# Kernel optimization log

Measured on AMD Instinct MI355X. Metric: run time of the kernel, lower is better.

## Reference

```python
import jax, jax.numpy as jnp
import numpy as np

N_NODES = 50000
N_EDGES = 800000
F_IN = 64
HIDDEN = 128
HEADS = 4
C = HIDDEN // HEADS  # 32 per-head channels
OUT = 256
N_GRAPHS = 1024
BN_EPS = 1e-5
SLOPE = 0.2  # PyG GATConv leaky_relu negative_slope default


def setup_inputs() -> dict:
    key = jax.random.key(0)
    ks = jax.random.split(key, 16)
    x = jax.random.normal(ks[0], (N_NODES, F_IN), dtype=jnp.float32)
    edge_index = jax.random.randint(ks[1], (2, N_EDGES), 0, N_NODES, dtype=jnp.int64)
    batch = jnp.sort(jax.random.randint(ks[2], (N_NODES,), 0, N_GRAPHS, dtype=jnp.int64))
    s = lambda *d: 1.0 / np.sqrt(d[0])
    W1 = jax.random.normal(ks[3], (F_IN, HIDDEN), dtype=jnp.float32) * s(F_IN)
    att_src1 = jax.random.normal(ks[4], (HEADS, C), dtype=jnp.float32) * s(C)
    att_dst1 = jax.random.normal(ks[5], (HEADS, C), dtype=jnp.float32) * s(C)
    b1 = jnp.zeros((HIDDEN,), jnp.float32)
    W2 = jax.random.normal(ks[6], (HIDDEN, HIDDEN), dtype=jnp.float32) * s(HIDDEN)
    att_src2 = jax.random.normal(ks[7], (HEADS, C), dtype=jnp.float32) * s(C)
    att_dst2 = jax.random.normal(ks[8], (HEADS, C), dtype=jnp.float32) * s(C)
    b2 = jnp.zeros((HIDDEN,), jnp.float32)
    bn1_g = jnp.ones((HIDDEN,), jnp.float32); bn1_b = jnp.zeros((HIDDEN,), jnp.float32)
    bn2_g = jnp.ones((HIDDEN,), jnp.float32); bn2_b = jnp.zeros((HIDDEN,), jnp.float32)
    Wlin = jax.random.normal(ks[9], (HIDDEN, OUT), dtype=jnp.float32) * s(HIDDEN)
    blin = jnp.zeros((OUT,), jnp.float32)
    return {"x": x, "edge_index": edge_index, "batch": batch,
            "W1": W1, "att_src1": att_src1, "att_dst1": att_dst1, "b1": b1,
            "W2": W2, "att_src2": att_src2, "att_dst2": att_dst2, "b2": b2,
            "bn1_g": bn1_g, "bn1_b": bn1_b, "bn2_g": bn2_g, "bn2_b": bn2_b,
            "Wlin": Wlin, "blin": blin}


def _gat_conv(x, W, a_src, a_dst, bias, src, dst):
    # x: [N, Fin] -> h: [N, H, C]
    h = (x @ W).reshape(-1, HEADS, C)
    e_src = jnp.sum(h * a_src, axis=-1)  # [N, H]
    e_dst = jnp.sum(h * a_dst, axis=-1)  # [N, H]
    e = jax.nn.leaky_relu(e_src[src] + e_dst[dst], SLOPE)  # [E, H]
    # scatter-softmax over edges grouped by destination node
    m = jax.ops.segment_max(e, dst, num_segments=N_NODES)
    ex = jnp.exp(e - m[dst])
    denom = jax.ops.segment_sum(ex, dst, num_segments=N_NODES)
    alpha = ex / (denom[dst] + 1e-16)  # [E, H]
    out = jax.ops.segment_sum(alpha[:, :, None] * h[src], dst, num_segments=N_NODES)
    return out.reshape(-1, HEADS * C) + bias


def _batchnorm(x, g, b):
    mu = jnp.mean(x, axis=0)
    var = jnp.var(x, axis=0)
    return (x - mu) * jax.lax.rsqrt(var + BN_EPS) * g + b


def reference(x, edge_index, batch, W1, att_src1, att_dst1, b1, W2, att_src2, att_dst2, b2,
              bn1_g, bn1_b, bn2_g, bn2_b, Wlin, blin):
    # PyG GATConv adds self-loops by default
    ar = jnp.arange(N_NODES, dtype=edge_index.dtype)
    src = jnp.concatenate([edge_index[0], ar])
    dst = jnp.concatenate([edge_index[1], ar])
    h = _gat_conv(x, W1, att_src1, att_dst1, b1, src, dst)
    h = jax.nn.elu(_batchnorm(h, bn1_g, bn1_b))
    h = _gat_conv(h, W2, att_src2, att_dst2, b2, src, dst)
    h = jax.nn.elu(_batchnorm(h, bn2_g, bn2_b))
    # global mean pool per graph
    sums = jax.ops.segment_sum(h, batch, num_segments=N_GRAPHS)
    cnts = jax.ops.segment_sum(jnp.ones((N_NODES,), h.dtype), batch, num_segments=N_GRAPHS)
    pooled = sums / jnp.maximum(cnts, 1.0)[:, None]  # [G, HIDDEN]
    return pooled @ Wlin + blin
```

## Files before the change

### kernel.cpp

```cpp
#include <hip/hip_runtime.h>
#include <hip/hip_bf16.h>
#include <hip/hip_fp16.h>
#include <math.h>

#define N_NODES 50000
#define N_EDGES 800000
#define E_TOT   (N_EDGES + N_NODES)
#define F_IN    64
#define HIDDEN  128
#define HEADS   4
#define OUT_DIM 256
#define N_GRAPHS 1024
#define BN_EPS  1e-5f
#define SLOPE   0.2f

#define SCAN_TILE 2048
#define N_TILES   ((N_NODES + SCAN_TILE - 1) / SCAN_TILE)
#define POOL_NODES 128
#define SCATTER_BLOCKS ((E_TOT + 1023) / 1024)
#define GEMM_BLOCKS    ((N_NODES + 63) / 64)


__global__ void hist_kernel(const int* __restrict__ ei, int* __restrict__ deg) {
    int base = blockIdx.x * blockDim.x * 4 + threadIdx.x;
    #pragma unroll
    for (int u = 0; u < 4; ++u) {
        int i = base + u * 256;
        if (i < E_TOT) {
            int d = (i < N_EDGES) ? ei[N_EDGES + i] : (i - N_EDGES);
            atomicAdd(&deg[d], 1);
        }
    }
}

__global__ void scan_partial_kernel(const int* __restrict__ deg, int* __restrict__ tile_sums) {
    __shared__ int wsum[4];
    int tile = blockIdx.x;
    int tid = threadIdx.x;
    int base = tile * SCAN_TILE + tid * 8;
    int s = 0;
    #pragma unroll
    for (int k = 0; k < 8; ++k) {
        int i = base + k;
        if (i < N_NODES) s += deg[i];
    }
    int lane = tid & 63;
    for (int off = 1; off < 64; off <<= 1) s += __shfl_xor(s, off, 64);
    if (lane == 0) wsum[tid >> 6] = s;
    __syncthreads();
    if (tid == 0) tile_sums[tile] = wsum[0] + wsum[1] + wsum[2] + wsum[3];
}

__global__ void scan_tilesums_kernel(const int* __restrict__ tile_sums, int* __restrict__ tile_off) {
    if (threadIdx.x == 0) {
        int acc = 0;
        for (int t = 0; t < N_TILES; ++t) { tile_off[t] = acc; acc += tile_sums[t]; }
    }
}

__global__ void scan_apply_kernel(const int* __restrict__ deg, const int* __restrict__ tile_off,
                                  int* __restrict__ row_start) {
    __shared__ int wsum[4];
    int tile = blockIdx.x;
    int tid = threadIdx.x;
    int lane = tid & 63;
    int wid = tid >> 6;
    int base = tile * SCAN_TILE + tid * 8;
    int v[8];
    int tsum = 0;
    #pragma unroll
    for (int k = 0; k < 8; ++k) {
        int i = base + k;
        v[k] = (i < N_NODES) ? deg[i] : 0;
        tsum += v[k];
    }
    int sc = tsum;
    for (int off = 1; off < 64; off <<= 1) {
        int t = __shfl_up(sc, off, 64);
        if (lane >= off) sc += t;
    }
    if (lane == 63) wsum[wid] = sc;
    __syncthreads();
    int woff = 0;
    for (int w = 0; w < 4; ++w) woff += (w < wid) ? wsum[w] : 0;
    __syncthreads();
    int toff = tile_off[tile] + woff + (sc - tsum);
    #pragma unroll
    for (int k = 0; k < 8; ++k) {
        int i = base + k;
        if (i < N_NODES) row_start[i] = toff;
        toff += v[k];
    }
    if (tile == 0 && tid == 0) row_start[N_NODES] = E_TOT;
}


__device__ __forceinline__ void scatter_body(const int* __restrict__ ei,
                                             const int* __restrict__ row_start,
                                             int* __restrict__ cursor,
                                             unsigned short* __restrict__ csr_src,
                                             int bid) {
    int base = bid * 1024 + threadIdx.x;
    int s[4], d[4];
    bool ok[4];
    #pragma unroll
    for (int u = 0; u < 4; ++u) {
        int i = base + u * 256;
        ok[u] = i < E_TOT;
        if (ok[u]) {
            if (i < N_EDGES) { s[u] = ei[i]; d[u] = ei[N_EDGES + i]; }
            else             { s[u] = i - N_EDGES; d[u] = s[u]; }
        }
    }
    int pos[4];
    #pragma unroll
    for (int u = 0; u < 4; ++u)
        if (ok[u]) pos[u] = atomicAdd(&cursor[d[u]], 1);
    #pragma unroll
    for (int u = 0; u < 4; ++u)
        if (ok[u]) csr_src[row_start[d[u]] + pos[u]] = (unsigned short)s[u];
}

template<int FIN>
__device__ __forceinline__ void gemm_att_body(
        const float* __restrict__ X, const float* __restrict__ W,
        const float* __restrict__ a_src, const float* __restrict__ a_dst,
        __half* __restrict__ H, float* __restrict__ es, float* __restrict__ ed,
        int bid, float* Wl) {
    int tid = threadIdx.x;
    for (int i = tid * 4; i < FIN * HIDDEN; i += 256 * 4) {
        *reinterpret_cast<float4*>(&Wl[i]) = *reinterpret_cast<const float4*>(&W[i]);
    }
    __syncthreads();

    int cg = tid & 15;
    int np = tid >> 4;
    int nb = bid * 64 + np * 4;
    int j0 = cg * 8;

    bool ok[4];
    const float* xp[4];
    #pragma unroll
    for (int t = 0; t < 4; ++t) {
        ok[t] = (nb + t) < N_NODES;
        xp[t] = X + (size_t)(ok[t] ? nb + t : 0) * FIN;
    }
    float acc[4][8];
    #pragma unroll
    for (int t = 0; t < 4; ++t)
        #pragma unroll
        for (int c = 0; c < 8; ++c) acc[t][c] = 0.f;

    for (int k = 0; k < FIN; k += 4) {
        float4 xa[4];
        #pragma unroll
        for (int t = 0; t < 4; ++t) xa[t] = *reinterpret_cast<const float4*>(xp[t] + k);
        #pragma unroll
        for (int kk = 0; kk < 4; ++kk) {
            const float4 wA = *reinterpret_cast<const float4*>(&Wl[(k + kk) * HIDDEN + j0]);
            const float4 wB = *reinterpret_cast<const float4*>(&Wl[(k + kk) * HIDDEN + j0 + 4]);
            #pragma unroll
            for (int t = 0; t < 4; ++t) {
                float xv = (kk == 0) ? xa[t].x : (kk == 1) ? xa[t].y : (kk == 2) ? xa[t].z : xa[t].w;
                acc[t][0] += xv * wA.x; acc[t][1] += xv * wA.y;
                acc[t][2] += xv * wA.z; acc[t][3] += xv * wA.w;
                acc[t][4] += xv * wB.x; acc[t][5] += xv * wB.y;
                acc[t][6] += xv * wB.z; acc[t][7] += xv * wB.w;
            }
        }
    }

    #pragma unroll
    for (int t = 0; t < 4; ++t) {
        int n = nb + t;
        if (ok[t]) {
            union { __half2 h2[4]; float4 f4; } pk;
            pk.h2[0] = __floats2half2_rn(acc[t][0], acc[t][1]);
            pk.h2[1] = __floats2half2_rn(acc[t][2], acc[t][3]);
            pk.h2[2] = __floats2half2_rn(acc[t][4], acc[t][5]);
            pk.h2[3] = __floats2half2_rn(acc[t][6], acc[t][7]);
            *reinterpret_cast<float4*>(H + (size_t)n * HIDDEN + j0) = pk.f4;
        }
        float vs = 0.f, vd = 0.f;
        #pragma unroll
        for (int c = 0; c < 8; ++c) {
            vs += acc[t][c] * a_src[j0 + c];
            vd += acc[t][c] * a_dst[j0 + c];
        }
        vs += __shfl_xor(vs, 1, 64); vs += __shfl_xor(vs, 2, 64);
        vd += __shfl_xor(vd, 1, 64); vd += __shfl_xor(vd, 2, 64);
        if ((cg & 3) == 0 && ok[t]) {
            int h = cg >> 2;
            es[n * HEADS + h] = vs;
            ed[n * HEADS + h] = vd;
        }
    }
}

__global__ __launch_bounds__(256) void scatter_gemm1_kernel(
        const int* __restrict__ ei, const int* __restrict__ row_start,
        int* __restrict__ cursor, unsigned short* __restrict__ csr_src,
        const float* __restrict__ X, const float* __restrict__ W,
        const float* __restrict__ a_src, const float* __restrict__ a_dst,
        __half* __restrict__ H, float* __restrict__ es, float* __restrict__ ed) {
    __shared__ float Wl[F_IN * HIDDEN];
    int bid = blockIdx.x;
    if (bid < SCATTER_BLOCKS) {
        scatter_body(ei, row_start, cursor, csr_src, bid);
    } else {
        gemm_att_body<F_IN>(X, W, a_src, a_dst, H, es, ed, bid - SCATTER_BLOCKS, Wl);
    }
}

__global__ __launch_bounds__(256) void gemm_att2_kernel(
        const float* __restrict__ X, const float* __restrict__ W,
        const float* __restrict__ a_src, const float* __restrict__ a_dst,
        __half* __restrict__ H, float* __restrict__ es, float* __restrict__ ed) {
    __shared__ float Wl[HIDDEN * HIDDEN];
    gemm_att_body<HIDDEN>(X, W, a_src, a_dst, H, es, ed, blockIdx.x, Wl);
}

__global__ void gat_aggregate_kernel(const __half* __restrict__ H, const float* __restrict__ es,
                                     const float* __restrict__ ed, const int* __restrict__ row_start,
                                     const unsigned short* __restrict__ csr_src,
                                     const float* __restrict__ bias,
                                     float* __restrict__ out) {
    int lane = threadIdx.x & 63;
    int n = blockIdx.x * 4 + (threadIdx.x >> 6);
    if (n >= N_NODES) return;
    int hid = lane >> 4;
    float edn = ed[n * HEADS + hid];
    int k0 = row_start[n], k1 = row_start[n + 1];
    const __half2* Hp = reinterpret_cast<const __half2*>(H);
    float dsum = 0.f, accx = 0.f, accy = 0.f;
    int k = k0;
    for (; k + 3 < k1; k += 4) {
        int s0 = csr_src[k];
        int s1 = csr_src[k + 1];
        int s2 = csr_src[k + 2];
        int s3 = csr_src[k + 3];
        float e0 = es[s0 * HEADS + hid];
        float e1 = es[s1 * HEADS + hid];
        float e2 = es[s2 * HEADS + hid];
        float e3 = es[s3 * HEADS + hid];
        __half2 h0 = Hp[(size_t)s0 * (HIDDEN / 2) + lane];
        __half2 h1 = Hp[(size_t)s1 * (HIDDEN / 2) + lane];
        __half2 h2 = Hp[(size_t)s2 * (HIDDEN / 2) + lane];
        __half2 h3 = Hp[(size_t)s3 * (HIDDEN / 2) + lane];
        e0 += edn; e1 += edn; e2 += edn; e3 += edn;
        e0 = fmaxf(e0, SLOPE * e0);
        e1 = fmaxf(e1, SLOPE * e1);
        e2 = fmaxf(e2, SLOPE * e2);
        e3 = fmaxf(e3, SLOPE * e3);
        float ex0 = __expf(e0);
        float ex1 = __expf(e1);
        float ex2 = __expf(e2);
        float ex3 = __expf(e3);
        float2 f0 = __half22float2(h0);
        float2 f1 = __half22float2(h1);
        float2 f2 = __half22float2(h2);
        float2 f3 = __half22float2(h3);
        dsum += (ex0 + ex1) + (ex2 + ex3);
        accx += ex0 * f0.x + ex1 * f1.x + ex2 * f2.x + ex3 * f3.x;
        accy += ex0 * f0.y + ex1 * f1.y + ex2 * f2.y + ex3 * f3.y;
    }
    for (; k < k1; ++k) {
        int s0 = csr_src[k];
        float e0 = es[s0 * HEADS + hid] + edn;
        __half2 h0 = Hp[(size_t)s0 * (HIDDEN / 2) + lane];
        e0 = fmaxf(e0, SLOPE * e0);
        float ex0 = __expf(e0);
        float2 f0 = __half22float2(h0);
        dsum += ex0;
        accx += ex0 * f0.x;
        accy += ex0 * f0.y;
    }
    float inv = 1.f / (dsum + 1e-16f);
    int j = 2 * lane;
    out[(size_t)n * HIDDEN + j]     = accx * inv + bias[j];
    out[(size_t)n * HIDDEN + j + 1] = accy * inv + bias[j + 1];
}

__global__ void bn_stats_kernel(const float* __restrict__ X, float* __restrict__ stats) {
    int c = threadIdx.x & 127;
    int r0 = blockIdx.x * 2 + (threadIdx.x >> 7);
    float s = 0.f, s2 = 0.f;
    for (int n = r0; n < N_NODES; n += gridDim.x * 2) {
        float v = X[(size_t)n * HIDDEN + c];
        s += v;
        s2 += v * v;
    }
    atomicAdd(&stats[c], s);
    atomicAdd(&stats[HIDDEN + c], s2);
}

__global__ void bn_apply_kernel(float* __restrict__ X, const float* __restrict__ stats,
                                const float* __restrict__ g, const float* __restrict__ b) {
    const float invN = 1.f / (float)N_NODES;
    int i = blockIdx.x * blockDim.x + threadIdx.x;
    const int total = N_NODES * HIDDEN;
    for (; i < total; i += gridDim.x * blockDim.x) {
        int c = i & 127;
        float mu = stats[c] * invN;
        float var = stats[HIDDEN + c] * invN - mu * mu;
        float v = (X[i] - mu) * rsqrtf(var + BN_EPS) * g[c] + b[c];
        X[i] = (v > 0.f) ? v : expm1f(v);
    }
}

__global__ __launch_bounds__(256) void bn_apply_pool_kernel(
        const float* __restrict__ X, const float* __restrict__ stats,
        const float* __restrict__ g, const float* __restrict__ b,
        const int* __restrict__ batch,
        float* __restrict__ psum, float* __restrict__ pcnt) {
    const float invN = 1.f / (float)N_NODES;
    int c = threadIdx.x & 127;
    int h = threadIdx.x >> 7;
    int n0 = blockIdx.x * POOL_NODES + h * (POOL_NODES / 2);
    int n1 = n0 + POOL_NODES / 2;
    if (n1 > N_NODES) n1 = N_NODES;
    if (n0 >= n1) return;
    float mu = stats[c] * invN;
    float var = stats[HIDDEN + c] * invN - mu * mu;
    float sc = rsqrtf(var + BN_EPS) * g[c];
    float sh = b[c] - mu * sc;
    int cur = batch[n0];
    float racc = 0.f, rcnt = 0.f;
    for (int n = n0; n < n1; ++n) {
        int gi = batch[n];
        if (gi != cur) {
            atomicAdd(&psum[cur * HIDDEN + c], racc);
            if (c == 0) atomicAdd(&pcnt[cur], rcnt);
            racc = 0.f; rcnt = 0.f; cur = gi;
        }
        float v = X[(size_t)n * HIDDEN + c] * sc + sh;
        v = (v > 0.f) ? v : expm1f(v);
        racc += v;
        rcnt += 1.f;
    }
    atomicAdd(&psum[cur * HIDDEN + c], racc);
    if (c == 0) atomicAdd(&pcnt[cur], rcnt);
}

__global__ void final_kernel(const float* __restrict__ psum, const float* __restrict__ pcnt,
                             const float* __restrict__ Wlin, const float* __restrict__ blin,
                             float* __restrict__ out) {
    int idx = blockIdx.x * blockDim.x + threadIdx.x;
    int g = idx >> 8, o = idx & 255;
    float invc = 1.f / fmaxf(pcnt[g], 1.f);
    float acc = blin[o];
    const float* pr = psum + g * HIDDEN;
    for (int j = 0; j < HIDDEN; ++j)
        acc += pr[j] * invc * Wlin[j * OUT_DIM + o];
    out[idx] = acc;
}


extern "C" void kernel_launch(void* const* d_in, const int* in_sizes, int n_in,
                              void* d_out, int out_size, void* d_ws, size_t ws_size,
                              hipStream_t stream) {
    const float* x    = (const float*)d_in[0];
    const int*   ei   = (const int*)d_in[1];
    const int*   batch= (const int*)d_in[2];
    const float* W1   = (const float*)d_in[3];
    const float* as1  = (const float*)d_in[4];
    const float* ad1  = (const float*)d_in[5];
    const float* b1   = (const float*)d_in[6];
    const float* W2   = (const float*)d_in[7];
    const float* as2  = (const float*)d_in[8];
    const float* ad2  = (const float*)d_in[9];
    const float* b2   = (const float*)d_in[10];
    const float* bn1g = (const float*)d_in[11];
    const float* bn1b = (const float*)d_in[12];
    const float* bn2g = (const float*)d_in[13];
    const float* bn2b = (const float*)d_in[14];
    const float* Wlin = (const float*)d_in[15];
    const float* blin = (const float*)d_in[16];
    float* out = (float*)d_out;

    char* ws = (char*)d_ws;
    const size_t SZ_H = (size_t)N_NODES * HIDDEN * 4;
    __half* A       = (__half*)(ws);
    float* B        = (float*)(ws + SZ_H);
    size_t off = 2 * SZ_H;
    float* es       = (float*)(ws + off); off += (size_t)N_NODES * HEADS * 4;
    float* ed       = (float*)(ws + off); off += (size_t)N_NODES * HEADS * 4;
    int*   row_start= (int*)(ws + off);   off += ((size_t)(N_NODES + 1) * 4 + 511) & ~511ull;
    unsigned short* csr_src = (unsigned short*)(ws + off);
    off += ((size_t)E_TOT * 2 + 511) & ~511ull;
    int*   tile_sums= (int*)(ws + off);   off += ((size_t)N_TILES * 4 + 511) & ~511ull;
    int*   tile_off = (int*)(ws + off);   off += ((size_t)N_TILES * 4 + 511) & ~511ull;
    size_t zoff = off;
    int*   deg      = (int*)(ws + off);   off += (size_t)N_NODES * 4;
    int*   cursor   = (int*)(ws + off);   off += (size_t)N_NODES * 4;
    float* stats1   = (float*)(ws + off); off += 2 * HIDDEN * 4;
    float* stats2   = (float*)(ws + off); off += 2 * HIDDEN * 4;
    float* psum     = (float*)(ws + off); off += (size_t)N_GRAPHS * HIDDEN * 4;
    float* pcnt     = (float*)(ws + off); off += (size_t)N_GRAPHS * 4;
    size_t zbytes = off - zoff;
    (void)ws_size; (void)n_in; (void)in_sizes; (void)out_size;

    hipMemsetAsync(ws + zoff, 0, zbytes, stream);

    const int TB = 256;
    const int egrid4 = SCATTER_BLOCKS;
    const int pgrid = (N_NODES + POOL_NODES - 1) / POOL_NODES;

    hist_kernel<<<egrid4, TB, 0, stream>>>(ei, deg);
    scan_partial_kernel<<<N_TILES, TB, 0, stream>>>(deg, tile_sums);
    scan_tilesums_kernel<<<1, 64, 0, stream>>>(tile_sums, tile_off);
    scan_apply_kernel<<<N_TILES, TB, 0, stream>>>(deg, tile_off, row_start);

    scatter_gemm1_kernel<<<SCATTER_BLOCKS + GEMM_BLOCKS, TB, 0, stream>>>(
        ei, row_start, cursor, csr_src, x, W1, as1, ad1, A, es, ed);

    gat_aggregate_kernel<<<N_NODES / 4, TB, 0, stream>>>(A, es, ed, row_start, csr_src, b1, B);
    bn_stats_kernel<<<512, TB, 0, stream>>>(B, stats1);
    bn_apply_kernel<<<2048, TB, 0, stream>>>(B, stats1, bn1g, bn1b);

    gemm_att2_kernel<<<GEMM_BLOCKS, TB, 0, stream>>>(B, W2, as2, ad2, A, es, ed);
    gat_aggregate_kernel<<<N_NODES / 4, TB, 0, stream>>>(A, es, ed, row_start, csr_src, b2, B);
    bn_stats_kernel<<<512, TB, 0, stream>>>(B, stats2);
    bn_apply_pool_kernel<<<pgrid, TB, 0, stream>>>(B, stats2, bn2g, bn2b, batch, psum, pcnt);

    final_kernel<<<(N_GRAPHS * OUT_DIM) / TB, TB, 0, stream>>>(psum, pcnt, Wlin, blin, out);
}
```

Measured before the change: 450.6 us.

## Store post-aggregation activations in fp16 and unroll edge gather by eight

The aggregation output buffer B becomes fp16 instead of fp32. The BN stats, BN apply, GEMM2 input and the pool kernels are rewritten to read and write half2 pairs, which halves the memory traffic of these bandwidth-bound passes. The edge loop in the aggregation kernel is unrolled from four to eight edges so more independent gathers are in flight. The cost is fp16 rounding of the normalized activations, which could reduce accuracy.

```diff
diff --git a/kernel.cpp b/kernel.cpp
--- a/kernel.cpp
+++ b/kernel.cpp
@@ -121,9 +121,9 @@
         if (ok[u]) csr_src[row_start[d[u]] + pos[u]] = (unsigned short)s[u];
 }
 
-template<int FIN>
+template<int FIN, bool XHALF>
 __device__ __forceinline__ void gemm_att_body(
-        const float* __restrict__ X, const float* __restrict__ W,
+        const void* __restrict__ Xv, const float* __restrict__ W,
         const float* __restrict__ a_src, const float* __restrict__ a_dst,
         __half* __restrict__ H, float* __restrict__ es, float* __restrict__ ed,
         int bid, float* Wl) {
@@ -139,11 +139,11 @@
     int j0 = cg * 8;
 
     bool ok[4];
-    const float* xp[4];
+    size_t rowb[4];
     #pragma unroll
     for (int t = 0; t < 4; ++t) {
         ok[t] = (nb + t) < N_NODES;
-        xp[t] = X + (size_t)(ok[t] ? nb + t : 0) * FIN;
+        rowb[t] = (size_t)(ok[t] ? nb + t : 0) * FIN;
     }
     float acc[4][8];
     #pragma unroll
@@ -153,8 +153,22 @@
 
     for (int k = 0; k < FIN; k += 4) {
         float4 xa[4];
-        #pragma unroll
-        for (int t = 0; t < 4; ++t) xa[t] = *reinterpret_cast<const float4*>(xp[t] + k);
+        if constexpr (XHALF) {
+            const __half* xb = (const __half*)Xv;
+            #pragma unroll
+            for (int t = 0; t < 4; ++t) {
+                union { float2 f2; __half2 h2[2]; } u;
+                u.f2 = *reinterpret_cast<const float2*>(xb + rowb[t] + k);
+                float2 a = __half22float2(u.h2[0]);
+                float2 c = __half22float2(u.h2[1]);
+                xa[t] = make_float4(a.x, a.y, c.x, c.y);
+            }
+        } else {
+            const float* xb = (const float*)Xv;
+            #pragma unroll
+            for (int t = 0; t < 4; ++t)
+                xa[t] = *reinterpret_cast<const float4*>(xb + rowb[t] + k);
+        }
         #pragma unroll
         for (int kk = 0; kk < 4; ++kk) {
             const float4 wA = *reinterpret_cast<const float4*>(&Wl[(k + kk) * HIDDEN + j0]);
@@ -208,23 +222,23 @@
     if (bid < SCATTER_BLOCKS) {
         scatter_body(ei, row_start, cursor, csr_src, bid);
     } else {
-        gemm_att_body<F_IN>(X, W, a_src, a_dst, H, es, ed, bid - SCATTER_BLOCKS, Wl);
+        gemm_att_body<F_IN, false>(X, W, a_src, a_dst, H, es, ed, bid - SCATTER_BLOCKS, Wl);
     }
 }
 
 __global__ __launch_bounds__(256) void gemm_att2_kernel(
-        const float* __restrict__ X, const float* __restrict__ W,
+        const __half* __restrict__ X, const float* __restrict__ W,
         const float* __restrict__ a_src, const float* __restrict__ a_dst,
         __half* __restrict__ H, float* __restrict__ es, float* __restrict__ ed) {
     __shared__ float Wl[HIDDEN * HIDDEN];
-    gemm_att_body<HIDDEN>(X, W, a_src, a_dst, H, es, ed, blockIdx.x, Wl);
+    gemm_att_body<HIDDEN, true>(X, W, a_src, a_dst, H, es, ed, blockIdx.x, Wl);
 }
 
 __global__ void gat_aggregate_kernel(const __half* __restrict__ H, const float* __restrict__ es,
                                      const float* __restrict__ ed, const int* __restrict__ row_start,
                                      const unsigned short* __restrict__ csr_src,
                                      const float* __restrict__ bias,
-                                     float* __restrict__ out) {
+                                     __half* __restrict__ out) {
     int lane = threadIdx.x & 63;
     int n = blockIdx.x * 4 + (threadIdx.x >> 6);
     if (n >= N_NODES) return;
@@ -234,35 +248,24 @@
     const __half2* Hp = reinterpret_cast<const __half2*>(H);
     float dsum = 0.f, accx = 0.f, accy = 0.f;
     int k = k0;
-    for (; k + 3 < k1; k += 4) {
-        int s0 = csr_src[k];
-        int s1 = csr_src[k + 1];
-        int s2 = csr_src[k + 2];
-        int s3 = csr_src[k + 3];
-        float e0 = es[s0 * HEADS + hid];
-        float e1 = es[s1 * HEADS + hid];
-        float e2 = es[s2 * HEADS + hid];
-        float e3 = es[s3 * HEADS + hid];
-        __half2 h0 = Hp[(size_t)s0 * (HIDDEN / 2) + lane];
-        __half2 h1 = Hp[(size_t)s1 * (HIDDEN / 2) + lane];
-        __half2 h2 = Hp[(size_t)s2 * (HIDDEN / 2) + lane];
-        __half2 h3 = Hp[(size_t)s3 * (HIDDEN / 2) + lane];
-        e0 += edn; e1 += edn; e2 += edn; e3 += edn;
-        e0 = fmaxf(e0, SLOPE * e0);
-        e1 = fmaxf(e1, SLOPE * e1);
-        e2 = fmaxf(e2, SLOPE * e2);
-        e3 = fmaxf(e3, SLOPE * e3);
-        float ex0 = __expf(e0);
-        float ex1 = __expf(e1);
-        float ex2 = __expf(e2);
-        float ex3 = __expf(e3);
-        float2 f0 = __half22float2(h0);
-        float2 f1 = __half22float2(h1);
-        float2 f2 = __half22float2(h2);
-        float2 f3 = __half22float2(h3);
-        dsum += (ex0 + ex1) + (ex2 + ex3);
-        accx += ex0 * f0.x + ex1 * f1.x + ex2 * f2.x + ex3 * f3.x;
-        accy += ex0 * f0.y + ex1 * f1.y + ex2 * f2.y + ex3 * f3.y;
+    for (; k + 7 < k1; k += 8) {
+        int s[8]; float e[8]; __half2 hh[8];
+        #pragma unroll
+        for (int u = 0; u < 8; ++u) s[u] = csr_src[k + u];
+        #pragma unroll
+        for (int u = 0; u < 8; ++u) e[u] = es[s[u] * HEADS + hid];
+        #pragma unroll
+        for (int u = 0; u < 8; ++u) hh[u] = Hp[(size_t)s[u] * (HIDDEN / 2) + lane];
+        #pragma unroll
+        for (int u = 0; u < 8; ++u) {
+            float ee = e[u] + edn;
+            ee = fmaxf(ee, SLOPE * ee);
+            float ex = __expf(ee);
+            float2 f = __half22float2(hh[u]);
+            dsum += ex;
+            accx += ex * f.x;
+            accy += ex * f.y;
+        }
     }
     for (; k < k1; ++k) {
         int s0 = csr_src[k];
@@ -277,69 +280,88 @@
     }
     float inv = 1.f / (dsum + 1e-16f);
     int j = 2 * lane;
-    out[(size_t)n * HIDDEN + j]     = accx * inv + bias[j];
-    out[(size_t)n * HIDDEN + j + 1] = accy * inv + bias[j + 1];
-}
-
-__global__ void bn_stats_kernel(const float* __restrict__ X, float* __restrict__ stats) {
-    int c = threadIdx.x & 127;
-    int r0 = blockIdx.x * 2 + (threadIdx.x >> 7);
-    float s = 0.f, s2 = 0.f;
-    for (int n = r0; n < N_NODES; n += gridDim.x * 2) {
-        float v = X[(size_t)n * HIDDEN + c];
-        s += v;
-        s2 += v * v;
-    }
-    atomicAdd(&stats[c], s);
-    atomicAdd(&stats[HIDDEN + c], s2);
-}
-
-__global__ void bn_apply_kernel(float* __restrict__ X, const float* __restrict__ stats,
+    reinterpret_cast<__half2*>(out)[(size_t)n * (HIDDEN / 2) + lane] =
+        __floats2half2_rn(accx * inv + bias[j], accy * inv + bias[j + 1]);
+}
+
+__global__ void bn_stats_kernel(const __half* __restrict__ X, float* __restrict__ stats) {
+    int cp = threadIdx.x & 63;
+    int rg = threadIdx.x >> 6;
+    const __half2* Xp = reinterpret_cast<const __half2*>(X);
+    float sx = 0.f, sy = 0.f, s2x = 0.f, s2y = 0.f;
+    for (int n = blockIdx.x * 4 + rg; n < N_NODES; n += gridDim.x * 4) {
+        float2 f = __half22float2(Xp[(size_t)n * (HIDDEN / 2) + cp]);
+        sx += f.x; sy += f.y;
+        s2x += f.x * f.x; s2y += f.y * f.y;
+    }
+    atomicAdd(&stats[2 * cp], sx);
+    atomicAdd(&stats[2 * cp + 1], sy);
+    atomicAdd(&stats[HIDDEN + 2 * cp], s2x);
+    atomicAdd(&stats[HIDDEN + 2 * cp + 1], s2y);
+}
+
+__global__ void bn_apply_kernel(__half* __restrict__ X, const float* __restrict__ stats,
                                 const float* __restrict__ g, const float* __restrict__ b) {
     const float invN = 1.f / (float)N_NODES;
+    __half2* Xp = reinterpret_cast<__half2*>(X);
     int i = blockIdx.x * blockDim.x + threadIdx.x;
-    const int total = N_NODES * HIDDEN;
+    const int total = N_NODES * (HIDDEN / 2);
     for (; i < total; i += gridDim.x * blockDim.x) {
-        int c = i & 127;
-        float mu = stats[c] * invN;
-        float var = stats[HIDDEN + c] * invN - mu * mu;
-        float v = (X[i] - mu) * rsqrtf(var + BN_EPS) * g[c] + b[c];
-        X[i] = (v > 0.f) ? v : expm1f(v);
+        int cp = i & 63;
+        int c0 = 2 * cp, c1 = c0 + 1;
+        float mu0 = stats[c0] * invN, mu1 = stats[c1] * invN;
+        float var0 = stats[HIDDEN + c0] * invN - mu0 * mu0;
+        float var1 = stats[HIDDEN + c1] * invN - mu1 * mu1;
+        float2 f = __half22float2(Xp[i]);
+        float v0 = (f.x - mu0) * rsqrtf(var0 + BN_EPS) * g[c0] + b[c0];
+        float v1 = (f.y - mu1) * rsqrtf(var1 + BN_EPS) * g[c1] + b[c1];
+        v0 = (v0 > 0.f) ? v0 : expm1f(v0);
+        v1 = (v1 > 0.f) ? v1 : expm1f(v1);
+        Xp[i] = __floats2half2_rn(v0, v1);
     }
 }
 
 __global__ __launch_bounds__(256) void bn_apply_pool_kernel(
-        const float* __restrict__ X, const float* __restrict__ stats,
+        const __half* __restrict__ X, const float* __restrict__ stats,
         const float* __restrict__ g, const float* __restrict__ b,
         const int* __restrict__ batch,
         float* __restrict__ psum, float* __restrict__ pcnt) {
     const float invN = 1.f / (float)N_NODES;
-    int c = threadIdx.x & 127;
-    int h = threadIdx.x >> 7;
-    int n0 = blockIdx.x * POOL_NODES + h * (POOL_NODES / 2);
-    int n1 = n0 + POOL_NODES / 2;
+    int cp = threadIdx.x & 63;
+    int h = threadIdx.x >> 6;
+    int n0 = blockIdx.x * POOL_NODES + h * (POOL_NODES / 4);
+    int n1 = n0 + POOL_NODES / 4;
     if (n1 > N_NODES) n1 = N_NODES;
     if (n0 >= n1) return;
-    float mu = stats[c] * invN;
-    float var = stats[HIDDEN + c] * invN - mu * mu;
-    float sc = rsqrtf(var + BN_EPS) * g[c];
-    float sh = b[c] - mu * sc;
+    const __half2* Xp = reinterpret_cast<const __half2*>(X);
+    int c0 = 2 * cp, c1 = c0 + 1;
+    float mu0 = stats[c0] * invN, mu1 = stats[c1] * invN;
+    float var0 = stats[HIDDEN + c0] * invN - mu0 * mu0;
+    float var1 = stats[HIDDEN + c1] * invN - mu1 * mu1;
+    float sc0 = rsqrtf(var0 + BN_EPS) * g[c0];
+    float sc1 = rsqrtf(var1 + BN_EPS) * g[c1];
+    float sh0 = b[c0] - mu0 * sc0;
+    float sh1 = b[c1] - mu1 * sc1;
     int cur = batch[n0];
-    float racc = 0.f, rcnt = 0.f;
+    float ra0 = 0.f, ra1 = 0.f, rcnt = 0.f;
     for (int n = n0; n < n1; ++n) {
         int gi = batch[n];
         if (gi != cur) {
-            atomicAdd(&psum[cur * HIDDEN + c], racc);
-            if (c == 0) atomicAdd(&pcnt[cur], rcnt);
-            racc = 0.f; rcnt = 0.f; cur = gi;
-        }
-        float v = X[(size_t)n * HIDDEN + c] * sc + sh;
-        v = (v > 0.f) ? v : expm1f(v);
-        racc += v;
-        rcnt += 1.f;
-    }
-    atomicAdd(&psum[cur * HIDDEN + c], racc);
-    if (c == 0) atomicAdd(&pcnt[cur], rcnt);
+            atomicAdd(&psum[cur * HIDDEN + c0], ra0);
+            atomicAdd(&psum[cur * HIDDEN + c1], ra1);
+            if (cp == 0) atomicAdd(&pcnt[cur], rcnt);
+            ra0 = 0.f; ra1 = 0.f; rcnt = 0.f; cur = gi;
+        }
+        float2 f = __half22float2(Xp[(size_t)n * (HIDDEN / 2) + cp]);
+        float v0 = f.x * sc0 + sh0;
+        float v1 = f.y * sc1 + sh1;
+        v0 = (v0 > 0.f) ? v0 : expm1f(v0);
+        v1 = (v1 > 0.f) ? v1 : expm1f(v1);
+        ra0 += v0; ra1 += v1; rcnt += 1.f;
+    }
+    atomicAdd(&psum[cur * HIDDEN + c0], ra0);
+    atomicAdd(&psum[cur * HIDDEN + c1], ra1);
+    if (cp == 0) atomicAdd(&pcnt[cur], rcnt);
 }
 
 __global__ void final_kernel(const float* __restrict__ psum, const float* __restrict__ pcnt,
@@ -381,7 +403,7 @@
     char* ws = (char*)d_ws;
     const size_t SZ_H = (size_t)N_NODES * HIDDEN * 4;
     __half* A       = (__half*)(ws);
-    float* B        = (float*)(ws + SZ_H);
+    __half* B       = (__half*)(ws + SZ_H);
     size_t off = 2 * SZ_H;
     float* es       = (float*)(ws + off); off += (size_t)N_NODES * HEADS * 4;
     float* ed       = (float*)(ws + off); off += (size_t)N_NODES * HEADS * 4;
@@ -403,10 +425,9 @@
     hipMemsetAsync(ws + zoff, 0, zbytes, stream);
 
     const int TB = 256;
-    const int egrid4 = SCATTER_BLOCKS;
     const int pgrid = (N_NODES + POOL_NODES - 1) / POOL_NODES;
 
-    hist_kernel<<<egrid4, TB, 0, stream>>>(ei, deg);
+    hist_kernel<<<SCATTER_BLOCKS, TB, 0, stream>>>(ei, deg);
     scan_partial_kernel<<<N_TILES, TB, 0, stream>>>(deg, tile_sums);
     scan_tilesums_kernel<<<1, 64, 0, stream>>>(tile_sums, tile_off);
     scan_apply_kernel<<<N_TILES, TB, 0, stream>>>(deg, tile_off, row_start);
```

Result: slower. 568.4 us (+26.1%).
